# Optimization experiments

Measured on AMD Instinct MI355X. Metric: run time of the kernel, lower is better.

## Reference

```python
import jax, jax.numpy as jnp
import numpy as np
import math

B, S, E, H = 4, 1024, 1024, 16
D = E // H
C = 1.0           # Poincare ball curvature
CS = math.sqrt(C)
EPS = 1e-7

def _sq(x):
    return jnp.sum(x * x, axis=-1, keepdims=True)

def expmap0(v):
    n = jnp.sqrt(jnp.clip(_sq(v), 1e-15))
    return jnp.tanh(CS * n) * v / (CS * n)

def logmap0(y):
    n = jnp.sqrt(jnp.clip(_sq(y), 1e-15))
    t = jnp.clip(CS * n, 0.0, 1.0 - 1e-6)
    return jnp.arctanh(t) * y / (CS * n)

def hlinear(x, z, r):
    # Poincare fully-connected layer (HNN++, Shimizu et al.), as in hypll HLinear
    lam = 2.0 / jnp.clip(1.0 - C * _sq(x), EPS)          # [..., 1] conformal factor
    zn = jnp.clip(jnp.linalg.norm(z, axis=0), 1e-15)     # [out]
    xz = x @ z                                           # [..., out]
    tcr = 2.0 * CS * r
    v = (2.0 * zn / CS) * jnp.arcsinh(CS * lam * xz / zn * jnp.cosh(tcr) - (lam - 1.0) * jnp.sinh(tcr))
    w = jnp.sinh(CS * v) / CS
    return w / (1.0 + jnp.sqrt(1.0 + C * jnp.sum(w * w, -1, keepdims=True)))

def _beta(a, b):
    return math.exp(math.lgamma(a) + math.lgamma(b) - math.lgamma(a + b))

def _forward(query, key, value, zq, bq, zk, bk, zv, bv):
    pq, pk, pv = hlinear(query, zq, bq), hlinear(key, zk, bk), hlinear(value, zv, bv)
    split = lambda x: x.reshape(B, S, H, D).transpose(0, 2, 1, 3)   # [B,H,S,D]
    q, k, v = split(pq), split(pk), split(pv)
    # attention_similarity: negative per-head pairwise Poincare distance (all heads vectorized)
    q2 = jnp.sum(q * q, -1)                              # [B,H,Sq]
    k2 = jnp.sum(k * k, -1)                              # [B,H,Sk]
    qk = jnp.einsum('bhqd,bhkd->bhqk', q, k)
    diff2 = jnp.clip(q2[..., :, None] + k2[..., None, :] - 2.0 * qk, 0.0)
    den = jnp.clip((1.0 - C * q2)[..., :, None] * (1.0 - C * k2)[..., None, :], EPS)
    dist = jnp.arccosh(jnp.clip(1.0 + 2.0 * C * diff2 / den, 1.0 + 1e-6)) / CS
    # attention_activation: softmax over keys
    w = jax.nn.softmax(-dist, axis=-1)                   # [B,H,Sq,Sk]
    # attention_midpoint: weighted gyromidpoint of values over keys
    lam = 2.0 / jnp.clip(1.0 - C * jnp.sum(v * v, -1), EPS)          # [B,H,Sk]
    num = jnp.einsum('bhqk,bhkd->bhqd', w * lam[..., None, :], v)
    dnm = jnp.clip(jnp.einsum('bhqk,bhk->bhq', jnp.abs(w), lam - 1.0), EPS)
    u = num / dnm[..., None]
    mid = u / (1.0 + jnp.sqrt(jnp.clip(1.0 - C * _sq(u), EPS)))      # (1/2) Mobius scalar mult
    # manifold.cat: beta-concatenation of heads (HNN++)
    scale = _beta(E / 2.0, 0.5) / _beta(D / 2.0, 0.5)
    tv = logmap0(mid) * scale                            # tangent at origin, [B,H,S,D]
    return expmap0(tv.transpose(0, 2, 1, 3).reshape(B, S, E))

def setup_inputs():
    key = jax.random.key(0)
    ks = jax.random.split(key, 9)
    mk = lambda k: expmap0(jax.random.normal(k, (B, S, E), jnp.float32) * (0.3 / math.sqrt(E)))
    zs = lambda k: jax.random.normal(k, (E, E), jnp.float32) / math.sqrt(E)
    bs = lambda k: jax.random.normal(k, (E,), jnp.float32) * 0.01
    return {"query": mk(ks[0]), "key": mk(ks[1]), "value": mk(ks[2]),
            "zq": zs(ks[3]), "bq": bs(ks[4]), "zk": zs(ks[5]), "bk": bs(ks[6]),
            "zv": zs(ks[7]), "bv": bs(ks[8])}

def reference(query, key, value, zq, bq, zk, bk, zv, bv):
    return _forward(query, key, value, zq, bq, zk, bk, zv, bv)
```

## Files before the change

kernel.cpp:

```cpp
#include <hip/hip_runtime.h>
#include <cmath>

#define EPSF 1e-7f

constexpr int B_ = 4, S_ = 1024, E_ = 1024, H_ = 16, D_ = 64;
constexpr int BS_ = B_ * S_;

typedef __attribute__((ext_vector_type(8))) short bf16x8;
typedef __attribute__((ext_vector_type(4))) float f32x4;

__device__ inline unsigned int fbits(float f) { union { float f; unsigned int u; } x; x.f = f; return x.u; }
__device__ inline float ubits(unsigned int u) { union { unsigned int u; float f; } x; x.u = u; return x.f; }

__device__ inline unsigned short f2bf(float f) {
  unsigned int u = fbits(f);
  unsigned int r = u + 0x7fffu + ((u >> 16) & 1u);
  return (unsigned short)(r >> 16);
}
__device__ inline float bf2f(unsigned short h) { return ubits(((unsigned int)h) << 16); }
__device__ inline float fastrcp(float x) { return __builtin_amdgcn_rcpf(x); }
__device__ inline float fastsqrt(float x) { return __builtin_amdgcn_sqrtf(x); }

__device__ __forceinline__ void async_ld16(const unsigned short* g, unsigned short* l) {
  __builtin_amdgcn_global_load_lds(
      (const __attribute__((address_space(1))) unsigned int*)g,
      (__attribute__((address_space(3))) unsigned int*)l, 16, 0, 0);
}

__device__ __forceinline__ unsigned int cvt_pk_bf16(float lo, float hi) {
  unsigned int r;
  asm("v_cvt_pk_bf16_f32 %0, %1, %2" : "=v"(r) : "v"(lo), "v"(hi));
  return r;
}
__device__ __forceinline__ void permlane32_swap(unsigned int &a, unsigned int &b) {
  asm("v_permlane32_swap_b32 %0, %1" : "+v"(a), "+v"(b));
}
__device__ __forceinline__ void permlane16_swap(unsigned int &a, unsigned int &b) {
  asm("v_permlane16_swap_b32 %0, %1" : "+v"(a), "+v"(b));
}

__global__ __launch_bounds__(256) void prep_kernel(
    const float* __restrict__ xq, const float* __restrict__ xk,
    const float* __restrict__ xv, unsigned short* __restrict__ Xbf,
    float* __restrict__ lamRow,
    const float* __restrict__ zq, const float* __restrict__ zk, const float* __restrict__ zv,
    unsigned short* __restrict__ BhiT, float* __restrict__ Zpart) {
  const int bid = blockIdx.x;
  const int tid = threadIdx.x;
  if (bid < 3 * BS_ / 4) {
    const int wid = tid >> 6, lane = tid & 63;
    const int row = bid * 4 + wid;
    const float* x = (row < BS_) ? xq : (row < 2 * BS_ ? xk : xv);
    const int r = row & (BS_ - 1);
    const float4* src = (const float4*)(x + (size_t)r * E_);
    float4 v[4];
    #pragma unroll
    for (int j = 0; j < 4; j++) v[j] = src[lane + 64 * j];
    float s = 0.f;
    #pragma unroll
    for (int j = 0; j < 4; j++)
      s += v[j].x * v[j].x + v[j].y * v[j].y + v[j].z * v[j].z + v[j].w * v[j].w;
    #pragma unroll
    for (int m = 1; m < 64; m <<= 1) s += __shfl_xor(s, m, 64);
    uint2* dst = (uint2*)(Xbf + (size_t)row * E_);
    #pragma unroll
    for (int j = 0; j < 4; j++) {
      uint2 p;
      p.x = (unsigned int)f2bf(v[j].x) | ((unsigned int)f2bf(v[j].y) << 16);
      p.y = (unsigned int)f2bf(v[j].z) | ((unsigned int)f2bf(v[j].w) << 16);
      dst[lane + 64 * j] = p;
    }
    if (lane == 0) lamRow[row] = 2.0f / fmaxf(1.0f - s, EPSF);
    return;
  }
  const int lid = bid - 3 * BS_ / 4;
  const int mat = lid >> 8;
  const int rem = lid & 255;
  const int ky = rem >> 4, nx = rem & 15;
  const float* z = mat == 0 ? zq : (mat == 1 ? zk : zv);
  const int k0 = ky * 64, n0 = nx * 64;
  __shared__ float t[64][65];
  __shared__ float sred[64][4];
  {
    int kr = tid >> 4, nc = (tid & 15) * 4;
    #pragma unroll
    for (int i = 0; i < 4; i++) {
      float4 vv = *(const float4*)(z + (size_t)(k0 + kr + i * 16) * E_ + n0 + nc);
      t[kr + i * 16][nc + 0] = vv.x;
      t[kr + i * 16][nc + 1] = vv.y;
      t[kr + i * 16][nc + 2] = vv.z;
      t[kr + i * 16][nc + 3] = vv.w;
    }
  }
  __syncthreads();
  int nr = tid >> 2, kc = (tid & 3) * 16;
  unsigned int ph[8];
  float ss = 0.f;
  #pragma unroll
  for (int p = 0; p < 8; p++) {
    float x0 = t[kc + 2 * p][nr], x1 = t[kc + 2 * p + 1][nr];
    ph[p] = (unsigned int)f2bf(x0) | ((unsigned int)f2bf(x1) << 16);
    ss += x0 * x0 + x1 * x1;
  }
  size_t off = (size_t)mat * E_ * E_ + (size_t)(n0 + nr) * E_ + k0 + kc;
  uint4* dh = (uint4*)(BhiT + off);
  dh[0] = make_uint4(ph[0], ph[1], ph[2], ph[3]);
  dh[1] = make_uint4(ph[4], ph[5], ph[6], ph[7]);
  sred[nr][tid & 3] = ss;
  __syncthreads();
  if (tid < 64) {
    float v = sred[tid][0] + sred[tid][1] + sred[tid][2] + sred[tid][3];
    Zpart[(size_t)(mat * 16 + ky) * E_ + n0 + tid] = v;
  }
}

__global__ __launch_bounds__(256, 3) void hlinear_mfma_kernel(
    const unsigned short* __restrict__ Xbf,
    const unsigned short* __restrict__ BhiT,
    const float* __restrict__ lamRow, const float* __restrict__ Zpart,
    const float* __restrict__ bq, const float* __restrict__ bk, const float* __restrict__ bv,
    unsigned short* __restrict__ Wbf) {
  const int fid = blockIdx.x;
  const int xcd = fid & 7, j = fid >> 3;
  const int n0 = (j & 7) * 128;
  const int gp = xcd * 12 + (j >> 3);
  const int mat = gp >> 5;
  const int m0 = (gp & 31) * 128;

  const unsigned short* xa = Xbf + (size_t)mat * BS_ * E_;
  const unsigned short* bh = BhiT + (size_t)mat * E_ * E_;

  __shared__ unsigned short LDSU[18432];
  __shared__ float chznS[128], shS[128], tznS[128];
  unsigned short* As = LDSU;
  unsigned short* Bh = LDSU + 8192;

  const int tid = threadIdx.x;
  const int wid = tid >> 6, lane = tid & 63, quad = lane >> 4, l16 = lane & 15;
  const int wm = (wid >> 1) * 64, wn = (wid & 1) * 64;

  if (tid < 128) {
    const int col = n0 + tid;
    float s = 0.f;
    #pragma unroll
    for (int ky = 0; ky < 16; ky++)
      s += Zpart[(size_t)(mat * 16 + ky) * E_ + col];
    float zn = fmaxf(sqrtf(s), 1e-15f);
    const float* bb = (mat == 0) ? bq : ((mat == 1) ? bk : bv);
    float rb = bb[col];
    chznS[tid] = coshf(2.f * rb) / zn;
    shS[tid] = sinhf(2.f * rb);
    tznS[tid] = 2.f * zn;
  }

  f32x4 acc[4][4];
  #pragma unroll
  for (int i = 0; i < 4; i++)
    #pragma unroll
    for (int jj = 0; jj < 4; jj++) acc[i][jj] = (f32x4){0.f, 0.f, 0.f, 0.f};

  const int lrow = lane >> 3;
  const int lcs = ((lane & 7) ^ lrow) * 8;
  const int xsw = (l16 & 7);

  for (int kt = 0; kt < E_ / 64; ++kt) {
    __syncthreads();
    const int kb = kt * 64 + lcs;
    #pragma unroll
    for (int c2 = 0; c2 < 4; c2++) {
      const int c = wid * 4 + c2;
      const int grow = c * 8 + lrow;
      async_ld16(xa + (size_t)(m0 + grow) * E_ + kb, As + c * 512);
      async_ld16(bh + (size_t)(n0 + grow) * E_ + kb, Bh + c * 512);
    }
    __syncthreads();
    #pragma unroll
    for (int h = 0; h < 2; h++) {
      bf16x8 a[4];
      #pragma unroll
      for (int mt = 0; mt < 4; mt++) {
        int row = wm + mt * 16 + l16;
        a[mt] = *(const bf16x8*)&As[row * 64 + (((h * 4 + quad) ^ xsw) * 8)];
      }
      #pragma unroll
      for (int nt = 0; nt < 4; nt++) {
        int row = wn + nt * 16 + l16;
        bf16x8 bhf = *(const bf16x8*)&Bh[row * 64 + (((h * 4 + quad) ^ xsw) * 8)];
        #pragma unroll
        for (int mt = 0; mt < 4; mt++)
          acc[mt][nt] = __builtin_amdgcn_mfma_f32_16x16x32_bf16(a[mt], bhf, acc[mt][nt], 0, 0, 0);
      }
    }
  }

  const float* lamP = lamRow + mat * BS_;
  float lamv[16];
  #pragma unroll
  for (int mt = 0; mt < 4; mt++)
    #pragma unroll
    for (int r = 0; r < 4; r++)
      lamv[mt * 4 + r] = lamP[m0 + wm + mt * 16 + quad * 4 + r];

  __syncthreads();
  unsigned short* epi = LDSU + wid * 4608;
  #pragma unroll
  for (int nt = 0; nt < 4; nt++) {
    int ci = wn + nt * 16 + l16;
    float chzn = chznS[ci];
    float sh = shS[ci];
    float tzn = tznS[ci];
    #pragma unroll
    for (int mt = 0; mt < 4; mt++) {
      #pragma unroll
      for (int r = 0; r < 4; r++) {
        float lam = lamv[mt * 4 + r];
        float arg = fmaf(lam * acc[mt][nt][r], chzn, -(lam - 1.f) * sh);
        float sq2 = sqrtf(fmaf(arg, arg, 1.f));
        float v = tzn * __logf(arg + sq2);
        float ev = __expf(v);
        float w = 0.5f * (ev - fastrcp(ev));
        epi[(mt * 16 + quad * 4 + r) * 72 + nt * 16 + l16] = f2bf(w);
      }
    }
  }
  unsigned short* gout = Wbf + (size_t)mat * BS_ * E_ + (size_t)(m0 + wm) * E_ + n0 + wn;
  const int rrow = lane >> 3, seg = lane & 7;
  #pragma unroll
  for (int i = 0; i < 8; i++) {
    int row = i * 8 + rrow;
    uint4 val = *(const uint4*)&epi[row * 72 + seg * 8];
    *(uint4*)(gout + (size_t)row * E_ + seg * 8) = val;
  }
}

__global__ __launch_bounds__(256) void norm_vtrans_kernel(
    const unsigned short* __restrict__ Wbf, unsigned short* __restrict__ Pbf,
    float* __restrict__ HN,
    unsigned short* __restrict__ KsG, unsigned short* __restrict__ lamMG,
    unsigned int* __restrict__ auxG, unsigned short* __restrict__ VtG) {
  const int bid = blockIdx.x;
  const int tid = threadIdx.x;
  if (bid < 2 * BS_ / 4) {
    const int wid = tid >> 6, lane = tid & 63;
    const int row = bid * 4 + wid;
    const unsigned short* w = Wbf + (size_t)row * E_;
    union { uint4 q[2]; unsigned short s[16]; } in;
    in.q[0] = ((const uint4*)w)[lane * 2];
    in.q[1] = ((const uint4*)w)[lane * 2 + 1];
    float wv[16];
    float s = 0.f;
    #pragma unroll
    for (int i = 0; i < 16; i++) { wv[i] = bf2f(in.s[i]); s += wv[i] * wv[i]; }
    #pragma unroll
    for (int m = 1; m < 64; m <<= 1) s += __shfl_xor(s, m, 64);
    float t = 1.f / (1.f + sqrtf(1.f + s));
    union { uint4 q[2]; unsigned short s[16]; } out;
    float rv[16];
    float hs = 0.f;
    #pragma unroll
    for (int i = 0; i < 16; i++) {
      unsigned short p = f2bf(wv[i] * t);
      out.s[i] = p;
      rv[i] = bf2f(p);
      hs += rv[i] * rv[i];
    }
    hs += __shfl_xor(hs, 1, 64);
    hs += __shfl_xor(hs, 2, 64);
    const int mat = row >= BS_ ? 1 : 0;
    const int r4 = row & (BS_ - 1);
    const int b = r4 >> 10, key = r4 & (S_ - 1);
    const int head = lane >> 2;
    const size_t bhS = ((size_t)(b * H_ + head)) * S_;
    if (mat == 0) {
      ((uint4*)(Pbf + (size_t)row * E_))[lane * 2] = out.q[0];
      ((uint4*)(Pbf + (size_t)row * E_))[lane * 2 + 1] = out.q[1];
      if ((lane & 3) == 0) HN[(size_t)r4 * H_ + head] = hs;
    } else {
      float c = fastrcp(1.f - hs);
      union { uint4 q[2]; unsigned short s[16]; } ks;
      #pragma unroll
      for (int i = 0; i < 16; i++) ks.s[i] = f2bf(rv[i] * c);
      unsigned short* dst = KsG + (bhS + key) * 64 + (lane & 3) * 16;
      ((uint4*)dst)[0] = ks.q[0];
      ((uint4*)dst)[1] = ks.q[1];
      if ((lane & 3) == 0)
        auxG[bhS + key] = (unsigned int)f2bf(c) | ((unsigned int)f2bf(c * hs) << 16);
    }
    return;
  }
  const int lid = bid - 2 * BS_ / 4;
  const int xcd = lid & 7, s2 = lid >> 3;
  const int g = xcd + 8 * (s2 >> 4);
  const int h = s2 & 15;
  const int b = g >> 4, st = g & 15;
  const unsigned short* wvbase = Wbf + (size_t)2 * BS_ * E_;
  __shared__ unsigned short T[64][72];
  __shared__ float tS[64];
  const int wid = tid >> 6, lane = tid & 63;
  #pragma unroll 1
  for (int kk = 0; kk < 16; ++kk) {
    const int key = wid * 16 + kk;
    const unsigned short* rowp = wvbase + (size_t)(b * S_ + st * 64 + key) * E_;
    union { uint4 q[2]; unsigned short s[16]; } in;
    in.q[0] = ((const uint4*)rowp)[lane * 2];
    in.q[1] = ((const uint4*)rowp)[lane * 2 + 1];
    float s = 0.f;
    #pragma unroll
    for (int i = 0; i < 16; i++) { float f = bf2f(in.s[i]); s += f * f; }
    #pragma unroll
    for (int m = 1; m < 64; m <<= 1) s += __shfl_xor(s, m, 64);
    if ((lane >> 2) == h) {
      *(uint4*)&T[key][(lane & 3) * 16] = in.q[0];
      *(uint4*)&T[key][(lane & 3) * 16 + 8] = in.q[1];
    }
    if (lane == 0) tS[key] = 1.f / (1.f + sqrtf(1.f + s));
  }
  __syncthreads();
  {
    const int kr = tid >> 2, lc = (tid & 3) * 16;
    const float t = tS[kr];
    float rv[16];
    float hp = 0.f;
    #pragma unroll
    for (int i = 0; i < 16; i++) {
      unsigned short p = f2bf(bf2f(T[kr][lc + i]) * t);
      rv[i] = bf2f(p);
      hp += rv[i] * rv[i];
    }
    hp += __shfl_xor(hp, 1, 64);
    hp += __shfl_xor(hp, 2, 64);
    float lam = 2.f / fmaxf(1.f - hp, EPSF);
    #pragma unroll
    for (int i = 0; i < 16; i++) T[kr][lc + i] = f2bf(rv[i] * lam);
    const size_t bhS = ((size_t)(b * H_ + h)) * S_;
    if ((tid & 3) == 0) lamMG[bhS + st * 64 + kr] = f2bf(lam - 1.f);
  }
  __syncthreads();
  {
    const int d = tid >> 2, sc = (tid & 3) * 16;
    unsigned int o[8];
    #pragma unroll
    for (int i = 0; i < 8; i++) {
      int s0 = sc + 2 * i;
      o[i] = (unsigned int)T[s0][d] | ((unsigned int)T[s0 + 1][d] << 16);
    }
    const size_t bhS = ((size_t)(b * H_ + h)) * S_;
    unsigned short* dst = VtG + bhS * 64 + (size_t)d * S_ + st * 64 + sc;
    ((uint4*)dst)[0] = make_uint4(o[0], o[1], o[2], o[3]);
    ((uint4*)dst)[1] = make_uint4(o[4], o[5], o[6], o[7]);
  }
}

__global__ __launch_bounds__(512) void attention_kernel(
    const unsigned short* __restrict__ Pbf, const float* __restrict__ HN,
    const unsigned short* __restrict__ KsG, const unsigned short* __restrict__ VtG,
    const unsigned short* __restrict__ lamMG, const unsigned int* __restrict__ auxG,
    float* __restrict__ TV, float scale) {
  const int fid = blockIdx.x;
  const int xcd = fid & 7, slot = fid >> 3;
  const int group = xcd + 8 * (slot >> 3);
  const int qt = slot & 7;
  const int h = group & 15, b = group >> 4;

  const unsigned short* pq = Pbf;
  const float* hnq = HN;

  const int tid = threadIdx.x;
  const int wid = tid >> 6, lane = tid & 63;
  const int quad = lane >> 4, l16 = lane & 15;

  __shared__ __align__(16) unsigned short Kl[2][8192];
  __shared__ __align__(16) unsigned short Vl[2][8192];
  __shared__ __align__(16) unsigned short lamL[1024];
  __shared__ __align__(16) unsigned int auxL[1024];

  const size_t bhS = (size_t)(b * H_ + h) * S_;
  const int lr = lane >> 3, cch = lane & 7;
  const int xsw = l16 & 7;
  const unsigned short* kbase = KsG + bhS * 64;
  const unsigned short* vbase = VtG + bhS * 64;
  const int srow = wid * 8 + lr;
  const int scc = ((cch ^ lr) * 8);

  async_ld16(kbase + (size_t)srow * 64 + scc, &Kl[0][wid * 512]);
  async_ld16(kbase + (size_t)(64 + srow) * 64 + scc, &Kl[0][4096 + wid * 512]);
  async_ld16(vbase + (size_t)srow * S_ + scc, &Vl[0][wid * 512]);
  async_ld16(vbase + (size_t)srow * S_ + 64 + scc, &Vl[0][4096 + wid * 512]);

  ((unsigned int*)lamL)[tid] = ((const unsigned int*)(lamMG + bhS))[tid];
  ((uint2*)auxL)[tid] = ((const uint2*)(auxG + bhS))[tid];

  const int qrow0 = qt * 128 + wid * 16;
  const size_t qgrow = ((size_t)(b * S_ + qrow0 + l16)) * E_ + h * 64;
  bf16x8 aq0r = *(const bf16x8*)(pq + qgrow + quad * 8);
  bf16x8 aq1r = *(const bf16x8*)(pq + qgrow + 32 + quad * 8);
  const float q2l = hnq[((size_t)(b * S_ + qrow0 + l16)) * H_ + h];
  const float al = 2.f * fastrcp(1.f - q2l);
  const float sc2 = -2.f * al;
  bf16x8 aq0, aq1;
  #pragma unroll
  for (int j = 0; j < 8; j++) {
    aq0[j] = (short)f2bf(bf2f((unsigned short)aq0r[j]) * sc2);
    aq1[j] = (short)f2bf(bf2f((unsigned short)aq1r[j]) * sc2);
  }
  const unsigned short ae0 = (quad == 0) ? f2bf(al * q2l) : 0;
  const unsigned short ae1 = (quad == 0) ? f2bf(al) : 0;
  const bf16x8 aex = (bf16x8){(short)ae0, (short)ae1, 0, 0, 0, 0, 0, 0};

  f32x4 accO[4];
  #pragma unroll
  for (int dt = 0; dt < 4; dt++) accO[dt] = (f32x4){0.f, 0.f, 0.f, 0.f};
  f32x4 accD = (f32x4){0.f, 0.f, 0.f, 0.f};

  asm volatile("s_waitcnt vmcnt(0) lgkmcnt(0)" ::: "memory");
  __builtin_amdgcn_s_barrier();

  const int NIT = S_ / 128;
  int buf = 0;
  #pragma unroll 1
  for (int it = 0; it < NIT; ++it) {
    if (it + 1 < NIT) {
      const int kr0 = (it + 1) * 128;
      async_ld16(kbase + (size_t)(kr0 + srow) * 64 + scc, &Kl[buf ^ 1][wid * 512]);
      async_ld16(kbase + (size_t)(kr0 + 64 + srow) * 64 + scc, &Kl[buf ^ 1][4096 + wid * 512]);
      async_ld16(vbase + (size_t)srow * S_ + kr0 + scc, &Vl[buf ^ 1][wid * 512]);
      async_ld16(vbase + (size_t)srow * S_ + kr0 + 64 + scc, &Vl[buf ^ 1][4096 + wid * 512]);
    }
    #pragma unroll
    for (int half = 0; half < 2; half++) {
      const int kt = it * 2 + half;
      const unsigned short* Kb = &Kl[buf][half * 4096];
      const unsigned short* Vb = &Vl[buf][half * 4096];

      unsigned int Wp[4][2];
      #pragma unroll
      for (int nt = 0; nt < 4; nt++) {
        const int krow = nt * 16 + l16;
        bf16x8 bk0 = *(const bf16x8*)&Kb[krow * 64 + ((quad ^ xsw) * 8)];
        bf16x8 bk1 = *(const bf16x8*)&Kb[krow * 64 + (((4 + quad) ^ xsw) * 8)];
        unsigned int av = (quad == 0) ? auxL[kt * 64 + krow] : 0u;
        bf16x8 bex = (bf16x8){(short)(av & 0xFFFF), (short)(av >> 16), 0, 0, 0, 0, 0, 0};
        f32x4 z = (f32x4){0.f, 0.f, 0.f, 0.f};
        f32x4 st = __builtin_amdgcn_mfma_f32_16x16x32_bf16(bex, aex, z, 0, 0, 0);
        st = __builtin_amdgcn_mfma_f32_16x16x32_bf16(bk0, aq0, st, 0, 0, 0);
        st = __builtin_amdgcn_mfma_f32_16x16x32_bf16(bk1, aq1, st, 0, 0, 0);
        float w[4];
        #pragma unroll
        for (int r2 = 0; r2 < 4; r2++) {
          float t = fmaxf(st[r2], 1e-6f);
          float A = 1.f + t;
          w[r2] = A - fastsqrt(fmaf(A, A, -1.f));
        }
        Wp[nt][0] = cvt_pk_bf16(w[0], w[1]);
        Wp[nt][1] = cvt_pk_bf16(w[2], w[3]);
      }
      unsigned int x00 = Wp[0][0], y00 = Wp[1][0];
      permlane32_swap(x00, y00); permlane16_swap(x00, y00);
      unsigned int x01 = Wp[0][1], y01 = Wp[1][1];
      permlane32_swap(x01, y01); permlane16_swap(x01, y01);
      unsigned int x10 = Wp[2][0], y10 = Wp[3][0];
      permlane32_swap(x10, y10); permlane16_swap(x10, y10);
      unsigned int x11 = Wp[2][1], y11 = Wp[3][1];
      permlane32_swap(x11, y11); permlane16_swap(x11, y11);
      union { unsigned int u[4]; bf16x8 v; } ap0u, ap1u;
      ap0u.u[0] = x00; ap0u.u[1] = x01; ap0u.u[2] = y00; ap0u.u[3] = y01;
      ap1u.u[0] = x10; ap1u.u[1] = x11; ap1u.u[2] = y10; ap1u.u[3] = y11;
      const bf16x8 ap0 = ap0u.v, ap1 = ap1u.v;

      #pragma unroll
      for (int dt = 0; dt < 4; dt++) {
        const int drow = dt * 16 + l16;
        bf16x8 bv0 = *(const bf16x8*)&Vb[drow * 64 + ((quad ^ xsw) * 8)];
        bf16x8 bv1 = *(const bf16x8*)&Vb[drow * 64 + (((4 + quad) ^ xsw) * 8)];
        accO[dt] = __builtin_amdgcn_mfma_f32_16x16x32_bf16(ap0, bv0, accO[dt], 0, 0, 0);
        accO[dt] = __builtin_amdgcn_mfma_f32_16x16x32_bf16(ap1, bv1, accO[dt], 0, 0, 0);
      }
      bf16x8 bl0 = *(const bf16x8*)&lamL[kt * 64 + quad * 8];
      bf16x8 bl1 = *(const bf16x8*)&lamL[kt * 64 + 32 + quad * 8];
      accD = __builtin_amdgcn_mfma_f32_16x16x32_bf16(ap0, bl0, accD, 0, 0, 0);
      accD = __builtin_amdgcn_mfma_f32_16x16x32_bf16(ap1, bl1, accD, 0, 0, 0);
    }

    asm volatile("s_waitcnt vmcnt(0)" ::: "memory");
    __builtin_amdgcn_s_barrier();
    buf ^= 1;
  }

  #pragma unroll
  for (int r2 = 0; r2 < 4; r2++) {
    float rdsum = fastrcp(accD[r2]);
    float uu[4];
    float su = 0.f;
    #pragma unroll
    for (int dt = 0; dt < 4; dt++) { uu[dt] = accO[dt][r2] * rdsum; su += uu[dt] * uu[dt]; }
    su += __shfl_xor(su, 1, 64);
    su += __shfl_xor(su, 2, 64);
    su += __shfl_xor(su, 4, 64);
    su += __shfl_xor(su, 8, 64);
    float g = fastrcp(1.f + fastsqrt(fmaxf(1.f - su, EPSF)));
    float n2 = fmaxf(su * g * g, 1e-15f);
    float n = fastsqrt(n2);
    float fac = atanhf(fminf(n, 1.f - 1e-6f)) * fastrcp(n) * g * scale;
    size_t orow = ((size_t)(b * S_ + qrow0 + quad * 4 + r2)) * E_ + h * 64 + l16;
    #pragma unroll
    for (int dt = 0; dt < 4; dt++) TV[orow + dt * 16] = fac * uu[dt];
  }
}

__global__ __launch_bounds__(256) void expmap_kernel(float* __restrict__ TV) {
  const int wid = threadIdx.x >> 6, lane = threadIdx.x & 63;
  const int row = blockIdx.x * 4 + wid;
  float* w = TV + (size_t)row * E_;
  float4 v[4];
  #pragma unroll
  for (int j = 0; j < 4; j++) v[j] = ((float4*)w)[lane + 64 * j];
  float s = 0.f;
  #pragma unroll
  for (int j = 0; j < 4; j++)
    s += v[j].x * v[j].x + v[j].y * v[j].y + v[j].z * v[j].z + v[j].w * v[j].w;
  #pragma unroll
  for (int m = 1; m < 64; m <<= 1) s += __shfl_xor(s, m, 64);
  float n = sqrtf(fmaxf(s, 1e-15f));
  float f = tanhf(n) / n;
  #pragma unroll
  for (int j = 0; j < 4; j++) {
    v[j].x *= f; v[j].y *= f; v[j].z *= f; v[j].w *= f;
    ((float4*)w)[lane + 64 * j] = v[j];
  }
}

extern "C" void kernel_launch(void* const* d_in, const int* in_sizes, int n_in,
                              void* d_out, int out_size, void* d_ws, size_t ws_size,
                              hipStream_t stream) {
  (void)in_sizes; (void)n_in; (void)out_size; (void)ws_size;
  const float* q  = (const float*)d_in[0];
  const float* k  = (const float*)d_in[1];
  const float* v  = (const float*)d_in[2];
  const float* zq = (const float*)d_in[3];
  const float* bq = (const float*)d_in[4];
  const float* zk = (const float*)d_in[5];
  const float* bk = (const float*)d_in[6];
  const float* zv = (const float*)d_in[7];
  const float* bv = (const float*)d_in[8];

  unsigned short* Wbf = (unsigned short*)d_ws;
  unsigned short* Pbf = Wbf + (size_t)3 * BS_ * E_;
  unsigned short* BhiT = Pbf;
  unsigned short* Xbf = Pbf + (size_t)3 * BS_ * E_;
  float* HN           = (float*)(Xbf + (size_t)3 * BS_ * E_);
  float* lamRow       = HN + (size_t)3 * BS_ * H_;
  float* Zpart        = lamRow + 3 * BS_;
  unsigned short* VtG = (unsigned short*)(Zpart + 48 * E_);
  unsigned short* KsG = VtG + (size_t)B_ * H_ * 64 * S_;
  unsigned short* lamMG = KsG + (size_t)B_ * H_ * S_ * 64;
  unsigned int* auxG  = (unsigned int*)(lamMG + (size_t)B_ * H_ * S_);
  float* out          = (float*)d_out;

  double lb1 = lgamma(E_ / 2.0) + lgamma(0.5) - lgamma(E_ / 2.0 + 0.5);
  double lb2 = lgamma(D_ / 2.0) + lgamma(0.5) - lgamma(D_ / 2.0 + 0.5);
  float scale = (float)exp(lb1 - lb2);

  hipLaunchKernelGGL(prep_kernel, dim3(3 * BS_ / 4 + 768), dim3(256), 0, stream,
                     q, k, v, Xbf, lamRow, zq, zk, zv, BhiT, Zpart);
  hipLaunchKernelGGL(hlinear_mfma_kernel, dim3(768), dim3(256), 0, stream,
                     Xbf, BhiT, lamRow, Zpart, bq, bk, bv, Wbf);
  hipLaunchKernelGGL(norm_vtrans_kernel, dim3(2 * BS_ / 4 + 1024), dim3(256), 0, stream,
                     Wbf, Pbf, HN, KsG, lamMG, auxG, VtG);
  hipLaunchKernelGGL(attention_kernel, dim3(512), dim3(512), 0, stream,
                     Pbf, HN, KsG, VtG, lamMG, auxG, out, scale);
  hipLaunchKernelGGL(expmap_kernel, dim3(BS_ / 4), dim3(256), 0, stream, out);
}
```

Before: 216.3 us.

## Merge five kernels into two persistent kernels with software grid barriers

Turns the prep, hlinear and norm/transpose kernels into device functions run by one persistent 768-block kernel, separated by atomic-counter grid barriers. The expmap pass is folded into the attention kernel after its own grid barrier. The aim is to remove launch gaps and per-kernel tail effects. The cost is relying on every block being co-resident (768 blocks at 3 per CU, 512 at 4 per CU), barrier spin overhead, a shared-memory size fixed by the largest stage, and an added memset launch.

```diff
diff --git a/kernel.cpp b/kernel.cpp
--- a/kernel.cpp
+++ b/kernel.cpp
@@ -21,6 +21,22 @@
 __device__ inline float fastrcp(float x) { return __builtin_amdgcn_rcpf(x); }
 __device__ inline float fastsqrt(float x) { return __builtin_amdgcn_sqrtf(x); }
 
+__device__ __forceinline__ void grid_barrier(unsigned* bar, unsigned nb) {
+  __syncthreads();
+  if (threadIdx.x == 0) {
+    __threadfence();
+    unsigned g0 = atomicAdd(&bar[1], 0u);
+    if (atomicAdd(&bar[0], 1u) == nb - 1u) {
+      atomicExch(&bar[0], 0u);
+      atomicAdd(&bar[1], 1u);
+    } else {
+      while (atomicAdd(&bar[1], 0u) == g0) { __builtin_amdgcn_s_sleep(2); }
+    }
+    __threadfence();
+  }
+  __syncthreads();
+}
+
 __device__ __forceinline__ void async_ld16(const unsigned short* g, unsigned short* l) {
   __builtin_amdgcn_global_load_lds(
       (const __attribute__((address_space(1))) unsigned int*)g,
@@ -39,14 +55,13 @@
   asm("v_permlane16_swap_b32 %0, %1" : "+v"(a), "+v"(b));
 }
 
-__global__ __launch_bounds__(256) void prep_kernel(
-    const float* __restrict__ xq, const float* __restrict__ xk,
-    const float* __restrict__ xv, unsigned short* __restrict__ Xbf,
-    float* __restrict__ lamRow,
-    const float* __restrict__ zq, const float* __restrict__ zk, const float* __restrict__ zv,
-    unsigned short* __restrict__ BhiT, float* __restrict__ Zpart) {
-  const int bid = blockIdx.x;
-  const int tid = threadIdx.x;
+
+__device__ __forceinline__ void prep_unit(
+    int bid, int tid,
+    const float* xq, const float* xk, const float* xv,
+    unsigned short* Xbf, float* lamRow,
+    const float* zq, const float* zk, const float* zv,
+    unsigned short* BhiT, float* Zpart, unsigned char* smem) {
   if (bid < 3 * BS_ / 4) {
     const int wid = tid >> 6, lane = tid & 63;
     const int row = bid * 4 + wid;
@@ -73,14 +88,14 @@
     if (lane == 0) lamRow[row] = 2.0f / fmaxf(1.0f - s, EPSF);
     return;
   }
+  float (*t)[65] = (float(*)[65])smem;
+  float (*sred)[4] = (float(*)[4])(smem + 16640);
   const int lid = bid - 3 * BS_ / 4;
   const int mat = lid >> 8;
   const int rem = lid & 255;
   const int ky = rem >> 4, nx = rem & 15;
   const float* z = mat == 0 ? zq : (mat == 1 ? zk : zv);
   const int k0 = ky * 64, n0 = nx * 64;
-  __shared__ float t[64][65];
-  __shared__ float sred[64][4];
   {
     int kr = tid >> 4, nc = (tid & 15) * 4;
     #pragma unroll
@@ -114,13 +129,19 @@
   }
 }
 
-__global__ __launch_bounds__(256, 3) void hlinear_mfma_kernel(
-    const unsigned short* __restrict__ Xbf,
-    const unsigned short* __restrict__ BhiT,
-    const float* __restrict__ lamRow, const float* __restrict__ Zpart,
-    const float* __restrict__ bq, const float* __restrict__ bk, const float* __restrict__ bv,
-    unsigned short* __restrict__ Wbf) {
-  const int fid = blockIdx.x;
+__device__ __forceinline__ void hlinear_unit(
+    int fid, int tid,
+    const unsigned short* Xbf, const unsigned short* BhiT,
+    const float* lamRow, const float* Zpart,
+    const float* bq, const float* bk, const float* bv,
+    unsigned short* Wbf, unsigned char* smem) {
+  unsigned short* LDSU = (unsigned short*)smem;
+  float* chznS = (float*)(smem + 36864);
+  float* shS = chznS + 128;
+  float* tznS = shS + 128;
+  unsigned short* As = LDSU;
+  unsigned short* Bh = LDSU + 8192;
+
   const int xcd = fid & 7, j = fid >> 3;
   const int n0 = (j & 7) * 128;
   const int gp = xcd * 12 + (j >> 3);
@@ -130,12 +151,6 @@
   const unsigned short* xa = Xbf + (size_t)mat * BS_ * E_;
   const unsigned short* bh = BhiT + (size_t)mat * E_ * E_;
 
-  __shared__ unsigned short LDSU[18432];
-  __shared__ float chznS[128], shS[128], tznS[128];
-  unsigned short* As = LDSU;
-  unsigned short* Bh = LDSU + 8192;
-
-  const int tid = threadIdx.x;
   const int wid = tid >> 6, lane = tid & 63, quad = lane >> 4, l16 = lane & 15;
   const int wm = (wid >> 1) * 64, wn = (wid & 1) * 64;
 
@@ -233,13 +248,11 @@
   }
 }
 
-__global__ __launch_bounds__(256) void norm_vtrans_kernel(
-    const unsigned short* __restrict__ Wbf, unsigned short* __restrict__ Pbf,
-    float* __restrict__ HN,
-    unsigned short* __restrict__ KsG, unsigned short* __restrict__ lamMG,
-    unsigned int* __restrict__ auxG, unsigned short* __restrict__ VtG) {
-  const int bid = blockIdx.x;
-  const int tid = threadIdx.x;
+__device__ __forceinline__ void normvt_unit(
+    int bid, int tid,
+    const unsigned short* Wbf, unsigned short* Pbf, float* HN,
+    unsigned short* KsG, unsigned short* lamMG, unsigned int* auxG,
+    unsigned short* VtG, unsigned char* smem) {
   if (bid < 2 * BS_ / 4) {
     const int wid = tid >> 6, lane = tid & 63;
     const int row = bid * 4 + wid;
@@ -288,14 +301,14 @@
     }
     return;
   }
+  unsigned short (*T)[72] = (unsigned short(*)[72])smem;
+  float* tS = (float*)(smem + 9216);
   const int lid = bid - 2 * BS_ / 4;
   const int xcd = lid & 7, s2 = lid >> 3;
   const int g = xcd + 8 * (s2 >> 4);
   const int h = s2 & 15;
   const int b = g >> 4, st = g & 15;
   const unsigned short* wvbase = Wbf + (size_t)2 * BS_ * E_;
-  __shared__ unsigned short T[64][72];
-  __shared__ float tS[64];
   const int wid = tid >> 6, lane = tid & 63;
   #pragma unroll 1
   for (int kk = 0; kk < 16; ++kk) {
@@ -351,11 +364,40 @@
   }
 }
 
-__global__ __launch_bounds__(512) void attention_kernel(
-    const unsigned short* __restrict__ Pbf, const float* __restrict__ HN,
-    const unsigned short* __restrict__ KsG, const unsigned short* __restrict__ VtG,
-    const unsigned short* __restrict__ lamMG, const unsigned int* __restrict__ auxG,
-    float* __restrict__ TV, float scale) {
+__global__ __launch_bounds__(256, 3) void mega1_kernel(
+    const float* xq, const float* xk, const float* xv,
+    unsigned short* Xbf, float* lamRow,
+    const float* zq, const float* zk, const float* zv,
+    unsigned short* BhiT, float* Zpart,
+    const float* bq, const float* bk, const float* bv,
+    unsigned short* Wbf,
+    unsigned short* Pbf, float* HN,
+    unsigned short* KsG, unsigned short* lamMG,
+    unsigned int* auxG, unsigned short* VtG,
+    unsigned* bar) {
+  __shared__ __align__(16) unsigned char SMEM[38400];
+  const int tid = threadIdx.x;
+  const int bid = blockIdx.x;
+  #pragma unroll 1
+  for (int i = 0; i < 5; i++) {
+    prep_unit(bid + 768 * i, tid, xq, xk, xv, Xbf, lamRow, zq, zk, zv, BhiT, Zpart, SMEM);
+    __syncthreads();
+  }
+  grid_barrier(bar, 768);
+  hlinear_unit(bid, tid, Xbf, BhiT, lamRow, Zpart, bq, bk, bv, Wbf, SMEM);
+  grid_barrier(bar, 768);
+  #pragma unroll 1
+  for (int i = 0; i < 4; i++) {
+    normvt_unit(bid + 768 * i, tid, Wbf, Pbf, HN, KsG, lamMG, auxG, VtG, SMEM);
+    __syncthreads();
+  }
+}
+
+__global__ __launch_bounds__(512, 4) void mega2_kernel(
+    const unsigned short* Pbf, const float* HN,
+    const unsigned short* KsG, const unsigned short* VtG,
+    const unsigned short* lamMG, const unsigned int* auxG,
+    float* TV, float scale, unsigned* bar) {
   const int fid = blockIdx.x;
   const int xcd = fid & 7, slot = fid >> 3;
   const int group = xcd + 8 * (slot >> 3);
@@ -505,27 +547,27 @@
     #pragma unroll
     for (int dt = 0; dt < 4; dt++) TV[orow + dt * 16] = fac * uu[dt];
   }
-}
-
-__global__ __launch_bounds__(256) void expmap_kernel(float* __restrict__ TV) {
-  const int wid = threadIdx.x >> 6, lane = threadIdx.x & 63;
-  const int row = blockIdx.x * 4 + wid;
-  float* w = TV + (size_t)row * E_;
-  float4 v[4];
-  #pragma unroll
-  for (int j = 0; j < 4; j++) v[j] = ((float4*)w)[lane + 64 * j];
-  float s = 0.f;
-  #pragma unroll
-  for (int j = 0; j < 4; j++)
-    s += v[j].x * v[j].x + v[j].y * v[j].y + v[j].z * v[j].z + v[j].w * v[j].w;
-  #pragma unroll
-  for (int m = 1; m < 64; m <<= 1) s += __shfl_xor(s, m, 64);
-  float n = sqrtf(fmaxf(s, 1e-15f));
-  float f = tanhf(n) / n;
-  #pragma unroll
-  for (int j = 0; j < 4; j++) {
-    v[j].x *= f; v[j].y *= f; v[j].z *= f; v[j].w *= f;
-    ((float4*)w)[lane + 64 * j] = v[j];
+
+  grid_barrier(bar, 512);
+  {
+    const int row = blockIdx.x * 8 + wid;
+    float* w = TV + (size_t)row * E_;
+    float4 v[4];
+    #pragma unroll
+    for (int j = 0; j < 4; j++) v[j] = ((float4*)w)[lane + 64 * j];
+    float s = 0.f;
+    #pragma unroll
+    for (int j = 0; j < 4; j++)
+      s += v[j].x * v[j].x + v[j].y * v[j].y + v[j].z * v[j].z + v[j].w * v[j].w;
+    #pragma unroll
+    for (int m = 1; m < 64; m <<= 1) s += __shfl_xor(s, m, 64);
+    float n = sqrtf(fmaxf(s, 1e-15f));
+    float f = tanhf(n) / n;
+    #pragma unroll
+    for (int j = 0; j < 4; j++) {
+      v[j].x *= f; v[j].y *= f; v[j].z *= f; v[j].w *= f;
+      ((float4*)w)[lane + 64 * j] = v[j];
+    }
   }
 }
 
@@ -554,19 +596,18 @@
   unsigned short* KsG = VtG + (size_t)B_ * H_ * 64 * S_;
   unsigned short* lamMG = KsG + (size_t)B_ * H_ * S_ * 64;
   unsigned int* auxG  = (unsigned int*)(lamMG + (size_t)B_ * H_ * S_);
+  unsigned* barWS     = (unsigned*)(auxG + (size_t)B_ * H_ * S_);
   float* out          = (float*)d_out;
 
   double lb1 = lgamma(E_ / 2.0) + lgamma(0.5) - lgamma(E_ / 2.0 + 0.5);
   double lb2 = lgamma(D_ / 2.0) + lgamma(0.5) - lgamma(D_ / 2.0 + 0.5);
   float scale = (float)exp(lb1 - lb2);
 
-  hipLaunchKernelGGL(prep_kernel, dim3(3 * BS_ / 4 + 768), dim3(256), 0, stream,
-                     q, k, v, Xbf, lamRow, zq, zk, zv, BhiT, Zpart);
-  hipLaunchKernelGGL(hlinear_mfma_kernel, dim3(768), dim3(256), 0, stream,
-                     Xbf, BhiT, lamRow, Zpart, bq, bk, bv, Wbf);
-  hipLaunchKernelGGL(norm_vtrans_kernel, dim3(2 * BS_ / 4 + 1024), dim3(256), 0, stream,
-                     Wbf, Pbf, HN, KsG, lamMG, auxG, VtG);
-  hipLaunchKernelGGL(attention_kernel, dim3(512), dim3(512), 0, stream,
-                     Pbf, HN, KsG, VtG, lamMG, auxG, out, scale);
-  hipLaunchKernelGGL(expmap_kernel, dim3(BS_ / 4), dim3(256), 0, stream, out);
-}
+  hipMemsetAsync((void*)barWS, 0, 4 * sizeof(unsigned), stream);
+
+  hipLaunchKernelGGL(mega1_kernel, dim3(768), dim3(256), 0, stream,
+                     q, k, v, Xbf, lamRow, zq, zk, zv, BhiT, Zpart,
+                     bq, bk, bv, Wbf, Pbf, HN, KsG, lamMG, auxG, VtG, barWS);
+  hipLaunchKernelGGL(mega2_kernel, dim3(512), dim3(512), 0, stream,
+                     Pbf, HN, KsG, VtG, lamMG, auxG, out, scale, barWS + 2);
+}
```

Result: slower. 449.1 us (+107.6%).
